# Kernel optimization log

Measured on AMD Instinct MI355X. Metric: run time of the kernel, lower is better.

## Reference

```python
import jax, jax.numpy as jnp
import numpy as np

EPS = 1e-7  # keras.backend.epsilon()
ROUTING_ITERS = 3


def squash(x, axis=-1):
    # squash(v) = (|v|^2 / (1+|v|^2)) * v/|v|
    sq = jnp.sum(jnp.square(x), axis=axis, keepdims=True)
    safe = jnp.sqrt(sq + EPS)
    return (sq / (1.0 + sq)) * (x / safe)


def setup_inputs() -> dict:
    key = jax.random.key(0)
    k1, k2 = jax.random.split(key)
    B, N_in, D_in = 32, 2048, 16
    N_out, D_out = 64, 32
    x = jax.random.normal(k1, (B, N_in, D_in), dtype=jnp.float32)
    # glorot-ish scale for transformation matrices
    W = jax.random.normal(k2, (N_in, N_out, D_out, D_in), dtype=jnp.float32) * 0.05
    bias = jnp.zeros((N_out, D_out), dtype=jnp.float32)
    return {"x": x, "W": W, "bias": bias}


def reference(x, W, bias):
    B = x.shape[0]
    N_in, N_out, D_out, D_in = W.shape
    # predictions u_hat[b,i,j,d] = sum_p W[i,j,d,p] * x[b,i,p]
    u_hat = jnp.einsum('bip,ijdp->bijd', x, W)  # (B, N_in, N_out, D_out)
    b_log = jnp.zeros((B, N_in, N_out), dtype=x.dtype)
    v = None
    for it in range(ROUTING_ITERS):
        c = jax.nn.softmax(b_log, axis=-1)                  # (B, N_in, N_out)
        s = jnp.einsum('bij,bijd->bjd', c, u_hat) + bias    # (B, N_out, D_out)
        v = squash(s, axis=-1)                              # (B, N_out, D_out)
        if it < ROUTING_ITERS - 1:
            b_log = b_log + jnp.einsum('bijd,bjd->bij', u_hat, v)
    return v
```

## Files before the change

kernel.cpp:

```cpp
#include <hip/hip_runtime.h>


#define B_   32
#define NI   2048
#define NO   64
#define DO_  32
#define DI   16
#define IC   16
#define WSTRIDE ((size_t)NO * DO_ * DI)

typedef __bf16 bf16x8 __attribute__((ext_vector_type(8)));
typedef float  f32x16 __attribute__((ext_vector_type(16)));
union U16B { uint4 u; bf16x8 v; };

__global__ __launch_bounds__(256) void convert_xT_kernel(const float* __restrict__ x,
                                                         __bf16* __restrict__ xT)
{
    const int idx = blockIdx.x * 256 + threadIdx.x;
    const int m = idx & 31;
    const int h = (idx >> 5) & 1;
    const int i = idx >> 6;
    const float4 f0 = *(const float4*)(x + ((size_t)m * NI + i) * DI + 8 * h);
    const float4 f1 = *(const float4*)(x + ((size_t)m * NI + i) * DI + 8 * h + 4);
    __bf16 o[8] = {(__bf16)f0.x, (__bf16)f0.y, (__bf16)f0.z, (__bf16)f0.w,
                   (__bf16)f1.x, (__bf16)f1.y, (__bf16)f1.z, (__bf16)f1.w};
    *(uint4*)(xT + (size_t)idx * 8) = *(uint4*)o;
}

__global__ __launch_bounds__(256) void passA_kernel(const float* __restrict__ W,
                                                    const __bf16* __restrict__ xT,
                                                    __bf16* __restrict__ Wb,
                                                    float* __restrict__ part)
{
    __shared__ float lds[4][1024];
    const int tid = threadIdx.x, lane = tid & 63, w = tid >> 6;
    const int j  = blockIdx.x & 63;
    const int ch = blockIdx.x >> 6;
    const int i0 = ch * 64 + w * IC;
    const int m  = lane & 31, h = lane >> 5;

    const size_t toff = (((size_t)i0 * NO + j) * DO_ + m) * DI + 8 * h;
    const float*  Wp  = W  + toff;
    __bf16*       Wbp = Wb + toff;
    const __bf16* xp  = xT + (size_t)i0 * 512 + lane * 8;

    f32x16 acc;
    #pragma unroll
    for (int r = 0; r < 16; ++r) acc[r] = 0.0f;

    #pragma unroll 4
    for (int ii = 0; ii < IC; ++ii) {
        const float4 w0 = ((const float4*)Wp)[0];
        const float4 w1 = ((const float4*)Wp)[1];
        U16B a;
        a.v[0] = (__bf16)w0.x; a.v[1] = (__bf16)w0.y; a.v[2] = (__bf16)w0.z; a.v[3] = (__bf16)w0.w;
        a.v[4] = (__bf16)w1.x; a.v[5] = (__bf16)w1.y; a.v[6] = (__bf16)w1.z; a.v[7] = (__bf16)w1.w;
        *(uint4*)Wbp = a.u;
        U16B b; b.u = *(const uint4*)xp;
        acc = __builtin_amdgcn_mfma_f32_32x32x16_bf16(a.v, b.v, acc, 0, 0, 0);
        Wp += WSTRIDE; Wbp += WSTRIDE; xp += 512;
    }

    #pragma unroll
    for (int r = 0; r < 16; ++r) {
        const int row = (r & 3) + 8 * (r >> 2) + 4 * h;
        lds[w][row * 32 + m] = acc[r];
    }
    __syncthreads();
    float* pb = part + ((size_t)ch * NO + j) * 1024;
    #pragma unroll
    for (int q = 0; q < 4; ++q) {
        const int idx = tid + 256 * q;
        pb[idx] = lds[0][idx] + lds[1][idx] + lds[2][idx] + lds[3][idx];
    }
}

__global__ __launch_bounds__(256) void s_kernel(const __bf16* __restrict__ Wb,
                                                const __bf16* __restrict__ xT,
                                                const float* __restrict__ c,
                                                float* __restrict__ part)
{
    __shared__ float lds[4][1024];
    const int tid = threadIdx.x, lane = tid & 63, w = tid >> 6;
    const int j  = blockIdx.x & 63;
    const int ch = blockIdx.x >> 6;
    const int i0 = ch * 64 + w * IC;
    const int m  = lane & 31, h = lane >> 5;

    const __bf16* Wp = Wb + (((size_t)i0 * NO + j) * DO_ + m) * DI + 8 * h;
    const __bf16* xp = xT + (size_t)i0 * 512 + lane * 8;
    const float*  cp = c  + (size_t)i0 * (NO * B_) + j * B_ + m;

    f32x16 acc;
    #pragma unroll
    for (int r = 0; r < 16; ++r) acc[r] = 0.0f;

    #pragma unroll 4
    for (int ii = 0; ii < IC; ++ii) {
        U16B a; a.u = *(const uint4*)Wp;
        U16B b; b.u = *(const uint4*)xp;
        const float cv = *cp;
        f32x16 z;
        #pragma unroll
        for (int r = 0; r < 16; ++r) z[r] = 0.0f;
        f32x16 u = __builtin_amdgcn_mfma_f32_32x32x16_bf16(a.v, b.v, z, 0, 0, 0);
        #pragma unroll
        for (int r = 0; r < 16; ++r) acc[r] = fmaf(cv, u[r], acc[r]);
        Wp += WSTRIDE; xp += 512; cp += NO * B_;
    }

    #pragma unroll
    for (int r = 0; r < 16; ++r) {
        const int row = (r & 3) + 8 * (r >> 2) + 4 * h;
        lds[w][row * 32 + m] = acc[r];
    }
    __syncthreads();
    float* pb = part + ((size_t)ch * NO + j) * 1024;
    #pragma unroll
    for (int q = 0; q < 4; ++q) {
        const int idx = tid + 256 * q;
        pb[idx] = lds[0][idx] + lds[1][idx] + lds[2][idx] + lds[3][idx];
    }
}

__global__ __launch_bounds__(256) void t_kernel(const __bf16* __restrict__ Wb,
                                                const __bf16* __restrict__ xT,
                                                const float* __restrict__ vT,
                                                float* __restrict__ t)
{
    const int tid = threadIdx.x, lane = tid & 63;
    const int wid = blockIdx.x * 4 + (tid >> 6);
    const int j   = wid & 63;
    const int i0  = (wid >> 6) * IC;
    const int m   = lane & 31, h = lane >> 5;

    const __bf16* Wp = Wb + (((size_t)i0 * NO + j) * DO_ + m) * DI + 8 * h;
    const __bf16* xp = xT + (size_t)i0 * 512 + lane * 8;

    float vr[16];
    #pragma unroll
    for (int r = 0; r < 16; ++r) {
        const int row = (r & 3) + 8 * (r >> 2) + 4 * h;
        vr[r] = vT[((size_t)j * DO_ + row) * B_ + m];
    }

    #pragma unroll 4
    for (int ii = 0; ii < IC; ++ii) {
        U16B a; a.u = *(const uint4*)Wp;
        U16B b; b.u = *(const uint4*)xp;
        f32x16 z;
        #pragma unroll
        for (int r = 0; r < 16; ++r) z[r] = 0.0f;
        f32x16 u = __builtin_amdgcn_mfma_f32_32x32x16_bf16(a.v, b.v, z, 0, 0, 0);

        float p0 = 0.f, p1 = 0.f, p2 = 0.f, p3 = 0.f;
        #pragma unroll
        for (int r = 0; r < 16; r += 4) {
            p0 = fmaf(u[r + 0], vr[r + 0], p0);
            p1 = fmaf(u[r + 1], vr[r + 1], p1);
            p2 = fmaf(u[r + 2], vr[r + 2], p2);
            p3 = fmaf(u[r + 3], vr[r + 3], p3);
        }
        float tp = (p0 + p1) + (p2 + p3);
        tp += __shfl_xor(tp, 32);
        if (h == 0) t[(size_t)(i0 + ii) * (NO * B_) + j * B_ + m] = tp;
        Wp += WSTRIDE; xp += 512;
    }
}

__global__ __launch_bounds__(256) void softmax_kernel(float* __restrict__ t)
{
    __shared__ float red[8][32];
    __shared__ float row_m[32];
    __shared__ float row_s[32];
    const int i = blockIdx.x;
    const int tid = threadIdx.x;
    const int b = tid & 31;
    const int g = tid >> 5;
    float* base = t + (size_t)i * (NO * B_);

    float tv[8];
    #pragma unroll
    for (int k = 0; k < 8; ++k) tv[k] = base[(g * 8 + k) * B_ + b];

    float m8 = tv[0];
    #pragma unroll
    for (int k = 1; k < 8; ++k) m8 = fmaxf(m8, tv[k]);
    red[g][b] = m8;
    __syncthreads();
    if (tid < 32) {
        float mm = red[0][tid];
        #pragma unroll
        for (int gg = 1; gg < 8; ++gg) mm = fmaxf(mm, red[gg][tid]);
        row_m[tid] = mm;
    }
    __syncthreads();
    const float mm = row_m[b];
    float e[8]; float ps = 0.f;
    #pragma unroll
    for (int k = 0; k < 8; ++k) { e[k] = __expf(tv[k] - mm); ps += e[k]; }
    __syncthreads();
    red[g][b] = ps;
    __syncthreads();
    if (tid < 32) {
        float ss = 0.f;
        #pragma unroll
        for (int gg = 0; gg < 8; ++gg) ss += red[gg][tid];
        row_s[tid] = 1.0f / ss;
    }
    __syncthreads();
    const float inv = row_s[b];
    #pragma unroll
    for (int k = 0; k < 8; ++k) base[(g * 8 + k) * B_ + b] = e[k] * inv;
}

__global__ __launch_bounds__(256) void squash_kernel(const float* __restrict__ part,
                                                     const float* __restrict__ bias,
                                                     const float* __restrict__ v0T,
                                                     float* __restrict__ out,
                                                     int mode, float prescale)
{
    __shared__ float red[8][32];
    __shared__ float scl[32];
    const int j = blockIdx.x;
    const int tid = threadIdx.x;
    const int b = tid & 31;
    const int g = tid >> 5;
    const int d0 = g * 4;

    float sv[4];
    #pragma unroll
    for (int q = 0; q < 4; ++q) {
        const float* p = part + (size_t)j * 1024 + (d0 + q) * 32 + b;
        float a = 0.f;
        #pragma unroll
        for (int ch = 0; ch < 32; ++ch) a += p[(size_t)ch * NO * 1024];
        sv[q] = a * prescale + bias[j * DO_ + d0 + q];
    }

    float p2s = 0.f;
    #pragma unroll
    for (int q = 0; q < 4; ++q) p2s = fmaf(sv[q], sv[q], p2s);
    red[g][b] = p2s;
    __syncthreads();
    if (tid < 32) {
        float n2 = 0.f;
        #pragma unroll
        for (int gg = 0; gg < 8; ++gg) n2 += red[gg][tid];
        scl[tid] = n2 / ((1.0f + n2) * sqrtf(n2 + 1e-7f));
    }
    __syncthreads();
    const float sc = scl[b];
    #pragma unroll
    for (int q = 0; q < 4; ++q) {
        const int d = d0 + q;
        const float vq = sv[q] * sc;
        if (mode == 0)      out[((size_t)j * DO_ + d) * B_ + b] = vq;
        else if (mode == 1) out[((size_t)j * DO_ + d) * B_ + b] =
                                v0T[((size_t)j * DO_ + d) * B_ + b] + vq;
        else                out[((size_t)b * NO + j) * DO_ + d] = vq;
    }
}

extern "C" void kernel_launch(void* const* d_in, const int* in_sizes, int n_in,
                              void* d_out, int out_size, void* d_ws, size_t ws_size,
                              hipStream_t stream)
{
    const float* x    = (const float*)d_in[0];
    const float* W    = (const float*)d_in[1];
    const float* bias = (const float*)d_in[2];
    float* out = (float*)d_out;

    char* ws = (char*)d_ws;
    __bf16* Wb   = (__bf16*)ws;
    __bf16* xT   = (__bf16*)(ws + (size_t)134217728);
    float*  t_buf= (float*) (ws + (size_t)134217728 + 2097152);
    float*  part = (float*) (ws + (size_t)134217728 + 2097152 + 16777216);
    float*  v0T  = (float*) (ws + (size_t)134217728 + 2097152 + 16777216 + 8388608);
    float*  vsT  = v0T + (size_t)NO * DO_ * B_;

    const dim3 tW(256);
    const dim3 gX(512), gP(2048), gSm(NI), gSq(NO);

    convert_xT_kernel<<<gX, tW, 0, stream>>>(x, xT);

    passA_kernel<<<gP, tW, 0, stream>>>(W, xT, Wb, part);
    squash_kernel<<<gSq, tW, 0, stream>>>(part, bias, nullptr, v0T, 0, 1.0f / 64.0f);

    t_kernel<<<gP, tW, 0, stream>>>(Wb, xT, v0T, t_buf);
    softmax_kernel<<<gSm, tW, 0, stream>>>(t_buf);
    s_kernel<<<gP, tW, 0, stream>>>(Wb, xT, t_buf, part);
    squash_kernel<<<gSq, tW, 0, stream>>>(part, bias, v0T, vsT, 1, 1.0f);

    t_kernel<<<gP, tW, 0, stream>>>(Wb, xT, vsT, t_buf);
    softmax_kernel<<<gSm, tW, 0, stream>>>(t_buf);
    s_kernel<<<gP, tW, 0, stream>>>(Wb, xT, t_buf, part);
    squash_kernel<<<gSq, tW, 0, stream>>>(part, bias, nullptr, out, 2, 1.0f);
}
```

Measured before the change: 520.3 us.

## Fuse squash into producer kernels via last-block atomic counters

```diff
diff --git a/kernel.cpp b/kernel.cpp
--- a/kernel.cpp
+++ b/kernel.cpp
@@ -11,12 +11,75 @@
 
 typedef __bf16 bf16x8 __attribute__((ext_vector_type(8)));
 typedef float  f32x16 __attribute__((ext_vector_type(16)));
+typedef float  f32x4v __attribute__((ext_vector_type(4)));
 union U16B { uint4 u; bf16x8 v; };
 
+__device__ __forceinline__ bool last_block(int* cnt, int idx, int tid, int arrivals)
+{
+    __shared__ int lastf;
+    __syncthreads();
+    if (tid == 0) {
+        __threadfence();
+        const int prev = atomicAdd(cnt + idx, 1);
+        lastf = (prev == arrivals - 1) ? 1 : 0;
+        if (lastf) __threadfence();
+    }
+    __syncthreads();
+    return lastf != 0;
+}
+
+__device__ __forceinline__ void squash_tail(const float* __restrict__ part,
+                                            const float* __restrict__ bias,
+                                            const float* __restrict__ v0T,
+                                            float* __restrict__ outp,
+                                            int j, int tid, int mode, float prescale)
+{
+    __shared__ float red[8][32];
+    __shared__ float scl[32];
+    const int b = tid & 31;
+    const int g = tid >> 5;
+    const int d0 = g * 4;
+
+    float sv[4];
+    #pragma unroll
+    for (int q = 0; q < 4; ++q) {
+        const float* p = part + (size_t)j * 1024 + (d0 + q) * 32 + b;
+        float a = 0.f;
+        #pragma unroll
+        for (int ch = 0; ch < 32; ++ch) a += p[(size_t)ch * NO * 1024];
+        sv[q] = a * prescale + bias[j * DO_ + d0 + q];
+    }
+
+    float p2s = 0.f;
+    #pragma unroll
+    for (int q = 0; q < 4; ++q) p2s = fmaf(sv[q], sv[q], p2s);
+    red[g][b] = p2s;
+    __syncthreads();
+    if (tid < 32) {
+        float n2 = 0.f;
+        #pragma unroll
+        for (int gg = 0; gg < 8; ++gg) n2 += red[gg][tid];
+        scl[tid] = n2 / ((1.0f + n2) * sqrtf(n2 + 1e-7f));
+    }
+    __syncthreads();
+    const float sc = scl[b];
+    #pragma unroll
+    for (int q = 0; q < 4; ++q) {
+        const int d = d0 + q;
+        const float vq = sv[q] * sc;
+        if (mode == 0)      outp[((size_t)j * DO_ + d) * B_ + b] = vq;
+        else if (mode == 1) outp[((size_t)j * DO_ + d) * B_ + b] =
+                                v0T[((size_t)j * DO_ + d) * B_ + b] + vq;
+        else                outp[((size_t)b * NO + j) * DO_ + d] = vq;
+    }
+}
+
 __global__ __launch_bounds__(256) void convert_xT_kernel(const float* __restrict__ x,
-                                                         __bf16* __restrict__ xT)
+                                                         __bf16* __restrict__ xT,
+                                                         int* __restrict__ cnt)
 {
     const int idx = blockIdx.x * 256 + threadIdx.x;
+    if (idx < 192) cnt[idx] = 0;
     const int m = idx & 31;
     const int h = (idx >> 5) & 1;
     const int i = idx >> 6;
@@ -30,7 +93,10 @@
 __global__ __launch_bounds__(256) void passA_kernel(const float* __restrict__ W,
                                                     const __bf16* __restrict__ xT,
                                                     __bf16* __restrict__ Wb,
-                                                    float* __restrict__ part)
+                                                    float* __restrict__ part,
+                                                    const float* __restrict__ bias,
+                                                    float* __restrict__ v0T,
+                                                    int* __restrict__ cnt)
 {
     __shared__ float lds[4][1024];
     const int tid = threadIdx.x, lane = tid & 63, w = tid >> 6;
@@ -50,11 +116,11 @@
 
     #pragma unroll 4
     for (int ii = 0; ii < IC; ++ii) {
-        const float4 w0 = ((const float4*)Wp)[0];
-        const float4 w1 = ((const float4*)Wp)[1];
+        const f32x4v w0 = __builtin_nontemporal_load((const f32x4v*)Wp);
+        const f32x4v w1 = __builtin_nontemporal_load((const f32x4v*)Wp + 1);
         U16B a;
-        a.v[0] = (__bf16)w0.x; a.v[1] = (__bf16)w0.y; a.v[2] = (__bf16)w0.z; a.v[3] = (__bf16)w0.w;
-        a.v[4] = (__bf16)w1.x; a.v[5] = (__bf16)w1.y; a.v[6] = (__bf16)w1.z; a.v[7] = (__bf16)w1.w;
+        a.v[0] = (__bf16)w0[0]; a.v[1] = (__bf16)w0[1]; a.v[2] = (__bf16)w0[2]; a.v[3] = (__bf16)w0[3];
+        a.v[4] = (__bf16)w1[0]; a.v[5] = (__bf16)w1[1]; a.v[6] = (__bf16)w1[2]; a.v[7] = (__bf16)w1[3];
         *(uint4*)Wbp = a.u;
         U16B b; b.u = *(const uint4*)xp;
         acc = __builtin_amdgcn_mfma_f32_32x32x16_bf16(a.v, b.v, acc, 0, 0, 0);
@@ -73,12 +139,20 @@
         const int idx = tid + 256 * q;
         pb[idx] = lds[0][idx] + lds[1][idx] + lds[2][idx] + lds[3][idx];
     }
+
+    if (last_block(cnt, j, tid, 32))
+        squash_tail(part, bias, nullptr, v0T, j, tid, 0, 1.0f / 64.0f);
 }
 
 __global__ __launch_bounds__(256) void s_kernel(const __bf16* __restrict__ Wb,
                                                 const __bf16* __restrict__ xT,
                                                 const float* __restrict__ c,
-                                                float* __restrict__ part)
+                                                float* __restrict__ part,
+                                                const float* __restrict__ bias,
+                                                const float* __restrict__ v0T,
+                                                float* __restrict__ outp,
+                                                int* __restrict__ cnt,
+                                                int mode, float prescale)
 {
     __shared__ float lds[4][1024];
     const int tid = threadIdx.x, lane = tid & 63, w = tid >> 6;
@@ -91,18 +165,15 @@
     const __bf16* xp = xT + (size_t)i0 * 512 + lane * 8;
     const float*  cp = c  + (size_t)i0 * (NO * B_) + j * B_ + m;
 
-    f32x16 acc;
-    #pragma unroll
-    for (int r = 0; r < 16; ++r) acc[r] = 0.0f;
+    f32x16 acc, z;
+    #pragma unroll
+    for (int r = 0; r < 16; ++r) { acc[r] = 0.0f; z[r] = 0.0f; }
 
     #pragma unroll 4
     for (int ii = 0; ii < IC; ++ii) {
         U16B a; a.u = *(const uint4*)Wp;
         U16B b; b.u = *(const uint4*)xp;
         const float cv = *cp;
-        f32x16 z;
-        #pragma unroll
-        for (int r = 0; r < 16; ++r) z[r] = 0.0f;
         f32x16 u = __builtin_amdgcn_mfma_f32_32x32x16_bf16(a.v, b.v, z, 0, 0, 0);
         #pragma unroll
         for (int r = 0; r < 16; ++r) acc[r] = fmaf(cv, u[r], acc[r]);
@@ -121,6 +192,9 @@
         const int idx = tid + 256 * q;
         pb[idx] = lds[0][idx] + lds[1][idx] + lds[2][idx] + lds[3][idx];
     }
+
+    if (last_block(cnt, j, tid, 32))
+        squash_tail(part, bias, v0T, outp, j, tid, mode, prescale);
 }
 
 __global__ __launch_bounds__(256) void t_kernel(const __bf16* __restrict__ Wb,
@@ -144,13 +218,14 @@
         vr[r] = vT[((size_t)j * DO_ + row) * B_ + m];
     }
 
+    f32x16 z;
+    #pragma unroll
+    for (int r = 0; r < 16; ++r) z[r] = 0.0f;
+
     #pragma unroll 4
     for (int ii = 0; ii < IC; ++ii) {
         U16B a; a.u = *(const uint4*)Wp;
         U16B b; b.u = *(const uint4*)xp;
-        f32x16 z;
-        #pragma unroll
-        for (int r = 0; r < 16; ++r) z[r] = 0.0f;
         f32x16 u = __builtin_amdgcn_mfma_f32_32x32x16_bf16(a.v, b.v, z, 0, 0, 0);
 
         float p0 = 0.f, p1 = 0.f, p2 = 0.f, p3 = 0.f;
@@ -214,54 +289,6 @@
     for (int k = 0; k < 8; ++k) base[(g * 8 + k) * B_ + b] = e[k] * inv;
 }
 
-__global__ __launch_bounds__(256) void squash_kernel(const float* __restrict__ part,
-                                                     const float* __restrict__ bias,
-                                                     const float* __restrict__ v0T,
-                                                     float* __restrict__ out,
-                                                     int mode, float prescale)
-{
-    __shared__ float red[8][32];
-    __shared__ float scl[32];
-    const int j = blockIdx.x;
-    const int tid = threadIdx.x;
-    const int b = tid & 31;
-    const int g = tid >> 5;
-    const int d0 = g * 4;
-
-    float sv[4];
-    #pragma unroll
-    for (int q = 0; q < 4; ++q) {
-        const float* p = part + (size_t)j * 1024 + (d0 + q) * 32 + b;
-        float a = 0.f;
-        #pragma unroll
-        for (int ch = 0; ch < 32; ++ch) a += p[(size_t)ch * NO * 1024];
-        sv[q] = a * prescale + bias[j * DO_ + d0 + q];
-    }
-
-    float p2s = 0.f;
-    #pragma unroll
-    for (int q = 0; q < 4; ++q) p2s = fmaf(sv[q], sv[q], p2s);
-    red[g][b] = p2s;
-    __syncthreads();
-    if (tid < 32) {
-        float n2 = 0.f;
-        #pragma unroll
-        for (int gg = 0; gg < 8; ++gg) n2 += red[gg][tid];
-        scl[tid] = n2 / ((1.0f + n2) * sqrtf(n2 + 1e-7f));
-    }
-    __syncthreads();
-    const float sc = scl[b];
-    #pragma unroll
-    for (int q = 0; q < 4; ++q) {
-        const int d = d0 + q;
-        const float vq = sv[q] * sc;
-        if (mode == 0)      out[((size_t)j * DO_ + d) * B_ + b] = vq;
-        else if (mode == 1) out[((size_t)j * DO_ + d) * B_ + b] =
-                                v0T[((size_t)j * DO_ + d) * B_ + b] + vq;
-        else                out[((size_t)b * NO + j) * DO_ + d] = vq;
-    }
-}
-
 extern "C" void kernel_launch(void* const* d_in, const int* in_sizes, int n_in,
                               void* d_out, int out_size, void* d_ws, size_t ws_size,
                               hipStream_t stream)
@@ -278,22 +305,22 @@
     float*  part = (float*) (ws + (size_t)134217728 + 2097152 + 16777216);
     float*  v0T  = (float*) (ws + (size_t)134217728 + 2097152 + 16777216 + 8388608);
     float*  vsT  = v0T + (size_t)NO * DO_ * B_;
+    int*    cnt  = (int*)  (ws + (size_t)162004992);
 
     const dim3 tW(256);
-    const dim3 gX(512), gP(2048), gSm(NI), gSq(NO);
-
-    convert_xT_kernel<<<gX, tW, 0, stream>>>(x, xT);
-
-    passA_kernel<<<gP, tW, 0, stream>>>(W, xT, Wb, part);
-    squash_kernel<<<gSq, tW, 0, stream>>>(part, bias, nullptr, v0T, 0, 1.0f / 64.0f);
+    const dim3 gX(512), gP(2048), gSm(NI);
+
+    convert_xT_kernel<<<gX, tW, 0, stream>>>(x, xT, cnt);
+
+    passA_kernel<<<gP, tW, 0, stream>>>(W, xT, Wb, part, bias, v0T, cnt);
 
     t_kernel<<<gP, tW, 0, stream>>>(Wb, xT, v0T, t_buf);
     softmax_kernel<<<gSm, tW, 0, stream>>>(t_buf);
-    s_kernel<<<gP, tW, 0, stream>>>(Wb, xT, t_buf, part);
-    squash_kernel<<<gSq, tW, 0, stream>>>(part, bias, v0T, vsT, 1, 1.0f);
+    s_kernel<<<gP, tW, 0, stream>>>(Wb, xT, t_buf, part, bias, v0T, vsT,
+                                    cnt + 64, 1, 1.0f);
 
     t_kernel<<<gP, tW, 0, stream>>>(Wb, xT, vsT, t_buf);
     softmax_kernel<<<gSm, tW, 0, stream>>>(t_buf);
-    s_kernel<<<gP, tW, 0, stream>>>(Wb, xT, t_buf, part);
-    squash_kernel<<<gSq, tW, 0, stream>>>(part, bias, nullptr, out, 2, 1.0f);
-}
+    s_kernel<<<gP, tW, 0, stream>>>(Wb, xT, t_buf, part, bias, nullptr, out,
+                                    cnt + 128, 2, 1.0f);
+}
```

Measured after the change: 732.1 us. 40.7% more time.

## Fuse agreement, softmax and weighted sum into one routing kernel

Applied to the files above, without the earlier changes.

```diff
diff --git a/kernel.cpp b/kernel.cpp
--- a/kernel.cpp
+++ b/kernel.cpp
@@ -75,150 +75,136 @@
     }
 }
 
-__global__ __launch_bounds__(256) void s_kernel(const __bf16* __restrict__ Wb,
-                                                const __bf16* __restrict__ xT,
-                                                const float* __restrict__ c,
-                                                float* __restrict__ part)
-{
-    __shared__ float lds[4][1024];
-    const int tid = threadIdx.x, lane = tid & 63, w = tid >> 6;
-    const int j  = blockIdx.x & 63;
-    const int ch = blockIdx.x >> 6;
-    const int i0 = ch * 64 + w * IC;
-    const int m  = lane & 31, h = lane >> 5;
-
-    const __bf16* Wp = Wb + (((size_t)i0 * NO + j) * DO_ + m) * DI + 8 * h;
-    const __bf16* xp = xT + (size_t)i0 * 512 + lane * 8;
-    const float*  cp = c  + (size_t)i0 * (NO * B_) + j * B_ + m;
-
-    f32x16 acc;
-    #pragma unroll
-    for (int r = 0; r < 16; ++r) acc[r] = 0.0f;
-
-    #pragma unroll 4
-    for (int ii = 0; ii < IC; ++ii) {
-        U16B a; a.u = *(const uint4*)Wp;
-        U16B b; b.u = *(const uint4*)xp;
-        const float cv = *cp;
-        f32x16 z;
-        #pragma unroll
-        for (int r = 0; r < 16; ++r) z[r] = 0.0f;
-        f32x16 u = __builtin_amdgcn_mfma_f32_32x32x16_bf16(a.v, b.v, z, 0, 0, 0);
-        #pragma unroll
-        for (int r = 0; r < 16; ++r) acc[r] = fmaf(cv, u[r], acc[r]);
-        Wp += WSTRIDE; xp += 512; cp += NO * B_;
-    }
-
-    #pragma unroll
-    for (int r = 0; r < 16; ++r) {
-        const int row = (r & 3) + 8 * (r >> 2) + 4 * h;
-        lds[w][row * 32 + m] = acc[r];
-    }
-    __syncthreads();
-    float* pb = part + ((size_t)ch * NO + j) * 1024;
-    #pragma unroll
-    for (int q = 0; q < 4; ++q) {
-        const int idx = tid + 256 * q;
-        pb[idx] = lds[0][idx] + lds[1][idx] + lds[2][idx] + lds[3][idx];
-    }
-}
-
-__global__ __launch_bounds__(256) void t_kernel(const __bf16* __restrict__ Wb,
-                                                const __bf16* __restrict__ xT,
-                                                const float* __restrict__ vT,
-                                                float* __restrict__ t)
-{
-    const int tid = threadIdx.x, lane = tid & 63;
-    const int wid = blockIdx.x * 4 + (tid >> 6);
-    const int j   = wid & 63;
-    const int i0  = (wid >> 6) * IC;
-    const int m   = lane & 31, h = lane >> 5;
-
-    const __bf16* Wp = Wb + (((size_t)i0 * NO + j) * DO_ + m) * DI + 8 * h;
-    const __bf16* xp = xT + (size_t)i0 * 512 + lane * 8;
-
-    float vr[16];
-    #pragma unroll
-    for (int r = 0; r < 16; ++r) {
-        const int row = (r & 3) + 8 * (r >> 2) + 4 * h;
-        vr[r] = vT[((size_t)j * DO_ + row) * B_ + m];
-    }
-
-    #pragma unroll 4
-    for (int ii = 0; ii < IC; ++ii) {
-        U16B a; a.u = *(const uint4*)Wp;
-        U16B b; b.u = *(const uint4*)xp;
-        f32x16 z;
-        #pragma unroll
-        for (int r = 0; r < 16; ++r) z[r] = 0.0f;
-        f32x16 u = __builtin_amdgcn_mfma_f32_32x32x16_bf16(a.v, b.v, z, 0, 0, 0);
-
-        float p0 = 0.f, p1 = 0.f, p2 = 0.f, p3 = 0.f;
-        #pragma unroll
-        for (int r = 0; r < 16; r += 4) {
-            p0 = fmaf(u[r + 0], vr[r + 0], p0);
-            p1 = fmaf(u[r + 1], vr[r + 1], p1);
-            p2 = fmaf(u[r + 2], vr[r + 2], p2);
-            p3 = fmaf(u[r + 3], vr[r + 3], p3);
-        }
-        float tp = (p0 + p1) + (p2 + p3);
-        tp += __shfl_xor(tp, 32);
-        if (h == 0) t[(size_t)(i0 + ii) * (NO * B_) + j * B_ + m] = tp;
-        Wp += WSTRIDE; xp += 512;
-    }
-}
-
-__global__ __launch_bounds__(256) void softmax_kernel(float* __restrict__ t)
-{
-    __shared__ float red[8][32];
+__global__ __launch_bounds__(512, 2) void fused_ts_kernel(const __bf16* __restrict__ Wb,
+                                                          const __bf16* __restrict__ xT,
+                                                          const float* __restrict__ vT,
+                                                          float* __restrict__ part)
+{
+    __shared__ float ct[64][32];
+    __shared__ float red[16][32];
     __shared__ float row_m[32];
     __shared__ float row_s[32];
-    const int i = blockIdx.x;
+
+    const int tid = threadIdx.x, lane = tid & 63, w = tid >> 6;
+    const int m = lane & 31, h = lane >> 5;
+    const int i0 = blockIdx.x * 8;
+    const int j0 = w * 8;
+    const int sb = tid & 31;
+    const int sg = tid >> 5;
+
+    f32x16 acc[8];
+    #pragma unroll
+    for (int jj = 0; jj < 8; ++jj) {
+        #pragma unroll
+        for (int r = 0; r < 16; ++r) acc[jj][r] = 0.0f;
+    }
+    f32x16 z;
+    #pragma unroll
+    for (int r = 0; r < 16; ++r) z[r] = 0.0f;
+
+    for (int ii = 0; ii < 8; ++ii) {
+        const int i = i0 + ii;
+        U16B xf; xf.u = *(const uint4*)(xT + (size_t)i * 512 + lane * 8);
+        const __bf16* Wbase = Wb + (((size_t)i * NO + j0) * DO_ + m) * DI + 8 * h;
+
+        #pragma unroll
+        for (int jj = 0; jj < 8; ++jj) {
+            U16B a; a.u = *(const uint4*)(Wbase + (size_t)jj * 512);
+            f32x16 u = __builtin_amdgcn_mfma_f32_32x32x16_bf16(a.v, xf.v, z, 0, 0, 0);
+            const float* vp = vT + ((size_t)(j0 + jj) * DO_ + 4 * h) * B_ + m;
+            float p0 = 0.f, p1 = 0.f, p2 = 0.f, p3 = 0.f;
+            #pragma unroll
+            for (int r = 0; r < 16; r += 4) {
+                const int ro = 8 * (r >> 2) * B_;
+                p0 = fmaf(u[r + 0], vp[ro + 0 * B_], p0);
+                p1 = fmaf(u[r + 1], vp[ro + 1 * B_], p1);
+                p2 = fmaf(u[r + 2], vp[ro + 2 * B_], p2);
+                p3 = fmaf(u[r + 3], vp[ro + 3 * B_], p3);
+            }
+            float tp = (p0 + p1) + (p2 + p3);
+            tp += __shfl_xor(tp, 32);
+            if (h == 0) ct[j0 + jj][m] = tp;
+        }
+        __syncthreads();
+
+        {
+            float tv[4];
+            #pragma unroll
+            for (int k = 0; k < 4; ++k) tv[k] = ct[sg * 4 + k][sb];
+            float m4 = fmaxf(fmaxf(tv[0], tv[1]), fmaxf(tv[2], tv[3]));
+            red[sg][sb] = m4;
+            __syncthreads();
+            if (tid < 32) {
+                float mm = red[0][tid];
+                #pragma unroll
+                for (int gg = 1; gg < 16; ++gg) mm = fmaxf(mm, red[gg][tid]);
+                row_m[tid] = mm;
+            }
+            __syncthreads();
+            const float mm = row_m[sb];
+            float ps = 0.f;
+            #pragma unroll
+            for (int k = 0; k < 4; ++k) {
+                const float e = __expf(tv[k] - mm);
+                ct[sg * 4 + k][sb] = e;
+                ps += e;
+            }
+            red[sg][sb] = ps;
+            __syncthreads();
+            if (tid < 32) {
+                float ss = 0.f;
+                #pragma unroll
+                for (int gg = 0; gg < 16; ++gg) ss += red[gg][tid];
+                row_s[tid] = 1.0f / ss;
+            }
+            __syncthreads();
+        }
+
+        const float inv = row_s[m];
+        #pragma unroll
+        for (int jj = 0; jj < 8; ++jj) {
+            U16B a; a.u = *(const uint4*)(Wbase + (size_t)jj * 512);
+            f32x16 u = __builtin_amdgcn_mfma_f32_32x32x16_bf16(a.v, xf.v, z, 0, 0, 0);
+            const float c = ct[j0 + jj][m] * inv;
+            #pragma unroll
+            for (int r = 0; r < 16; ++r) acc[jj][r] = fmaf(c, u[r], acc[jj][r]);
+        }
+        __syncthreads();
+    }
+
+    float* pb = part + ((size_t)blockIdx.x * NO + j0) * 1024;
+    #pragma unroll
+    for (int jj = 0; jj < 8; ++jj) {
+        #pragma unroll
+        for (int r = 0; r < 16; ++r) {
+            const int row = (r & 3) + 8 * (r >> 2) + 4 * h;
+            pb[jj * 1024 + row * 32 + m] = acc[jj][r];
+        }
+    }
+}
+
+__global__ __launch_bounds__(256) void reduce_kernel(const float* __restrict__ partF,
+                                                     float* __restrict__ partR)
+{
+    const int j  = blockIdx.x & 63;
+    const int cg = blockIdx.x >> 6;
     const int tid = threadIdx.x;
-    const int b = tid & 31;
-    const int g = tid >> 5;
-    float* base = t + (size_t)i * (NO * B_);
-
-    float tv[8];
-    #pragma unroll
-    for (int k = 0; k < 8; ++k) tv[k] = base[(g * 8 + k) * B_ + b];
-
-    float m8 = tv[0];
-    #pragma unroll
-    for (int k = 1; k < 8; ++k) m8 = fmaxf(m8, tv[k]);
-    red[g][b] = m8;
-    __syncthreads();
-    if (tid < 32) {
-        float mm = red[0][tid];
-        #pragma unroll
-        for (int gg = 1; gg < 8; ++gg) mm = fmaxf(mm, red[gg][tid]);
-        row_m[tid] = mm;
-    }
-    __syncthreads();
-    const float mm = row_m[b];
-    float e[8]; float ps = 0.f;
-    #pragma unroll
-    for (int k = 0; k < 8; ++k) { e[k] = __expf(tv[k] - mm); ps += e[k]; }
-    __syncthreads();
-    red[g][b] = ps;
-    __syncthreads();
-    if (tid < 32) {
-        float ss = 0.f;
-        #pragma unroll
-        for (int gg = 0; gg < 8; ++gg) ss += red[gg][tid];
-        row_s[tid] = 1.0f / ss;
-    }
-    __syncthreads();
-    const float inv = row_s[b];
-    #pragma unroll
-    for (int k = 0; k < 8; ++k) base[(g * 8 + k) * B_ + b] = e[k] * inv;
+    #pragma unroll
+    for (int q = 0; q < 4; ++q) {
+        const int idx = tid + 256 * q;
+        const float* p = partF + (((size_t)cg * 64) * NO + j) * 1024 + idx;
+        float a = 0.f;
+        #pragma unroll 8
+        for (int k = 0; k < 64; ++k) a += p[(size_t)k * NO * 1024];
+        partR[((size_t)cg * NO + j) * 1024 + idx] = a;
+    }
 }
 
 __global__ __launch_bounds__(256) void squash_kernel(const float* __restrict__ part,
                                                      const float* __restrict__ bias,
                                                      const float* __restrict__ v0T,
                                                      float* __restrict__ out,
-                                                     int mode, float prescale)
+                                                     int mode, float prescale, int nch)
 {
     __shared__ float red[8][32];
     __shared__ float scl[32];
@@ -233,8 +219,8 @@
     for (int q = 0; q < 4; ++q) {
         const float* p = part + (size_t)j * 1024 + (d0 + q) * 32 + b;
         float a = 0.f;
-        #pragma unroll
-        for (int ch = 0; ch < 32; ++ch) a += p[(size_t)ch * NO * 1024];
+        #pragma unroll 8
+        for (int ch = 0; ch < nch; ++ch) a += p[(size_t)ch * NO * 1024];
         sv[q] = a * prescale + bias[j * DO_ + d0 + q];
     }
 
@@ -272,28 +258,27 @@
     float* out = (float*)d_out;
 
     char* ws = (char*)d_ws;
-    __bf16* Wb   = (__bf16*)ws;
-    __bf16* xT   = (__bf16*)(ws + (size_t)134217728);
-    float*  t_buf= (float*) (ws + (size_t)134217728 + 2097152);
-    float*  part = (float*) (ws + (size_t)134217728 + 2097152 + 16777216);
-    float*  v0T  = (float*) (ws + (size_t)134217728 + 2097152 + 16777216 + 8388608);
-    float*  vsT  = v0T + (size_t)NO * DO_ * B_;
-
-    const dim3 tW(256);
-    const dim3 gX(512), gP(2048), gSm(NI), gSq(NO);
+    __bf16* Wb    = (__bf16*)ws;
+    __bf16* xT    = (__bf16*)(ws + (size_t)134217728);
+    float*  partP = (float*) (ws + (size_t)136314880);
+    float*  partF = (float*) (ws + (size_t)144703488);
+    float*  partR = (float*) (ws + (size_t)211812352);
+    float*  v0T   = (float*) (ws + (size_t)212860928);
+    float*  vsT   = (float*) (ws + (size_t)213123072);
+
+    const dim3 tW(256), tF(512);
+    const dim3 gX(512), gP(2048), gF(256), gR(256), gSq(NO);
 
     convert_xT_kernel<<<gX, tW, 0, stream>>>(x, xT);
 
-    passA_kernel<<<gP, tW, 0, stream>>>(W, xT, Wb, part);
-    squash_kernel<<<gSq, tW, 0, stream>>>(part, bias, nullptr, v0T, 0, 1.0f / 64.0f);
-
-    t_kernel<<<gP, tW, 0, stream>>>(Wb, xT, v0T, t_buf);
-    softmax_kernel<<<gSm, tW, 0, stream>>>(t_buf);
-    s_kernel<<<gP, tW, 0, stream>>>(Wb, xT, t_buf, part);
-    squash_kernel<<<gSq, tW, 0, stream>>>(part, bias, v0T, vsT, 1, 1.0f);
-
-    t_kernel<<<gP, tW, 0, stream>>>(Wb, xT, vsT, t_buf);
-    softmax_kernel<<<gSm, tW, 0, stream>>>(t_buf);
-    s_kernel<<<gP, tW, 0, stream>>>(Wb, xT, t_buf, part);
-    squash_kernel<<<gSq, tW, 0, stream>>>(part, bias, nullptr, out, 2, 1.0f);
-}
+    passA_kernel<<<gP, tW, 0, stream>>>(W, xT, Wb, partP);
+    squash_kernel<<<gSq, tW, 0, stream>>>(partP, bias, nullptr, v0T, 0, 1.0f / 64.0f, 32);
+
+    fused_ts_kernel<<<gF, tF, 0, stream>>>(Wb, xT, v0T, partF);
+    reduce_kernel<<<gR, tW, 0, stream>>>(partF, partR);
+    squash_kernel<<<gSq, tW, 0, stream>>>(partR, bias, v0T, vsT, 1, 1.0f, 4);
+
+    fused_ts_kernel<<<gF, tF, 0, stream>>>(Wb, xT, vsT, partF);
+    reduce_kernel<<<gR, tW, 0, stream>>>(partF, partR);
+    squash_kernel<<<gSq, tW, 0, stream>>>(partR, bias, nullptr, out, 2, 1.0f, 4);
+}
```

Result: slower. 805.2 us (+54.8%).
